# Performance work log

Measured on AMD Instinct MI355X. Metric: run time of the kernel, lower is better.

The kernel has to match this reference:

```python
import jax, jax.numpy as jnp
import numpy as np

B, T, C, L = 256, 512, 512, 64  # batch, timesteps, num_classes (blank = C-1), max label len
NEG = -1e30   # log-space 'minus infinity' that is safe under fp arithmetic
EPS = 1e-7    # keras.backend.epsilon() used by ctc_batch_cost


def _ctc_loss(log_probs, labels, in_len, lab_len, blank):
    """CTC negative log-likelihood via the forward (alpha) DP in log space.
    log_probs: [T, B, C] log probabilities; labels: [B, L] int; in_len, lab_len: [B] int.
    Returns [B] loss. Matches tf.nn.ctc_loss with merge_repeated=True, blank=C-1."""
    Tn, Bn, Cn = log_probs.shape
    Ln = labels.shape[1]
    S = 2 * Ln + 1  # extended label: blank, l1, blank, l2, ..., blank
    ext = jnp.full((Bn, S), blank, dtype=labels.dtype).at[:, 1::2].set(labels)  # [B,S]
    # skip transition s-2 -> s allowed iff ext[s] != blank and ext[s] != ext[s-2]
    allow = jnp.concatenate(
        [jnp.zeros((Bn, 2), dtype=bool),
         (ext[:, 2:] != blank) & (ext[:, 2:] != ext[:, :-2])], axis=1)  # [B,S]
    # emission log-probs for each extended-label position at every step: [T,B,S]
    emit = log_probs[:, jnp.arange(Bn)[:, None], ext]

    alpha0 = (jnp.full((Bn, S), NEG, dtype=log_probs.dtype)
              .at[:, 0].set(emit[0, :, 0])
              .at[:, 1].set(emit[0, :, 1]))

    def step(alpha, e):
        a1 = jnp.pad(alpha, ((0, 0), (1, 0)), constant_values=NEG)[:, :-1]
        a2 = jnp.pad(alpha, ((0, 0), (2, 0)), constant_values=NEG)[:, :-2]
        a2 = jnp.where(allow, a2, NEG)
        new = jax.nn.logsumexp(jnp.stack([alpha, a1, a2], axis=0), axis=0) + e
        return new, new

    _, alphas = jax.lax.scan(step, alpha0, emit[1:])
    alphas = jnp.concatenate([alpha0[None], alphas], axis=0)  # [T,B,S]
    # alpha at the last valid timestep of each sample
    final = alphas[in_len - 1, jnp.arange(Bn)]  # [B,S]
    i1 = (2 * lab_len)[:, None]       # last blank position
    i2 = (2 * lab_len - 1)[:, None]   # last label position
    last = jnp.concatenate(
        [jnp.take_along_axis(final, i1, axis=1),
         jnp.take_along_axis(final, i2, axis=1)], axis=1)  # [B,2]
    return -jax.nn.logsumexp(last, axis=1)  # [B]


def setup_inputs() -> dict:
    key = jax.random.key(0)
    k1, k2 = jax.random.split(key)
    # model output is a softmax distribution over classes (keras ctc_batch_cost contract)
    y_pred = jax.nn.softmax(jax.random.normal(k1, (B, T, C), dtype=jnp.float32), axis=-1)
    y_true = jax.random.randint(k2, (B, L), 0, C - 1, dtype=jnp.int32)  # never blank (C-1)
    input_length = jnp.full((B, 1), T, dtype=jnp.int32)
    label_length = jnp.full((B, 1), L, dtype=jnp.int32)
    return {"y_true": y_true, "y_pred": y_pred,
            "input_length": input_length, "label_length": label_length}


def reference(y_true, y_pred, input_length, label_length):
    # keras.backend.ctc_batch_cost: log(transpose(y_pred) + eps), blank = num_classes-1
    log_probs = jnp.log(jnp.transpose(y_pred, (1, 0, 2)) + EPS)  # [T,B,C]
    loss = _ctc_loss(log_probs, y_true, input_length[:, 0], label_length[:, 0], C - 1)
    return loss[:, None]  # [B,1], matching ctc_batch_cost
```

## Files before the change

### kernel.cpp

```cpp
#include <hip/hip_runtime.h>


constexpr int Bc = 256, Tc = 512, Cc = 512, Lc = 64;
constexpr int BLANK = Cc - 1;
constexpr float EPSF = 1e-7f;
constexpr float NEGI = -1e30f;
constexpr float LN2 = 0.6931471805599453f;
constexpr int K = 16;
constexpr int NC = (Tc - 1 + K - 1) / K;

__device__ __forceinline__ float exp2_hw(float x) { return __builtin_amdgcn_exp2f(x); }
__device__ __forceinline__ float log2_hw(float x) { return __builtin_amdgcn_logf(x); }

__device__ __forceinline__ float lse2(float a, float b) {
    float m = fmaxf(a, b);
    return m + log2_hw(exp2_hw(a - m) + exp2_hw(b - m));
}
__device__ __forceinline__ float lse3(float a, float b, float c) {
    float m = fmaxf(fmaxf(a, b), c);
    return m + log2_hw(exp2_hw(a - m) + exp2_hw(b - m) + exp2_hw(c - m));
}

__global__ __launch_bounds__(64, 1) void ctc_fwd(
    const int* __restrict__ labels,
    const float* __restrict__ yp,
    const int* __restrict__ in_len,
    const int* __restrict__ lab_len,
    float* __restrict__ out)
{
    const int b = blockIdx.x;
    const int lane = threadIdx.x;

    const float* __restrict__ row0 = yp + (size_t)b * (size_t)(Tc * Cc);

    const int lab = labels[b * Lc + lane];
    const int labPrev = __shfl_up(lab, 1);
    const bool allow = (lane >= 1 && lab != BLANK && lab != labPrev);

    int til = in_len[b];  if (til > Tc) til = Tc;
    const int lln = lab_len[b];

    float aB, aL, aH = NEGI;
    {
        float eb0 = log2_hw(row0[BLANK] + EPSF);
        float el0 = log2_hw(row0[lab] + EPSF);
        aB = (lane == 0) ? eb0 : NEGI;
        aL = (lane == 0) ? el0 : NEGI;
    }

    float curL[K], curB[K], nxtL[K], nxtB[K];

    auto loadChunk = [&](int c, float* dL, float* dB) {
        #pragma unroll
        for (int k = 0; k < K; ++k) {
            int t = 1 + c * K + k;
            bool v = (t < Tc);
            size_t o = (size_t)t * Cc;
            dL[k] = v ? row0[o + lab]   : 1.0f;
            dB[k] = v ? row0[o + BLANK] : 1.0f;
        }
    };

    loadChunk(0, curL, curB);

    for (int c = 0; c < NC; ++c) {
        if (c + 1 < NC) loadChunk(c + 1, nxtL, nxtB);

        #pragma unroll
        for (int k = 0; k < K; ++k) {
            int t = 1 + c * K + k;
            float el = log2_hw(curL[k] + EPSF);
            float eb = log2_hw(curB[k] + EPSF);

            float lp = __shfl_up(aL, 1);
            lp = (lane == 0) ? NEGI : lp;
            float lpm = allow ? lp : NEGI;

            float nB = lse2(aB, lp) + eb;
            float nL = lse3(aL, aB, lpm) + el;
            float nH = lse2(aH, aL) + eb;
            if (t < til) { aB = nB; aL = nL; aH = nH; }
        }

        #pragma unroll
        for (int k = 0; k < K; ++k) { curL[k] = nxtL[k]; curB[k] = nxtB[k]; }
    }

    float v1a = __shfl(aB, lln & 63);
    float v1b = __shfl(aH, 63);
    float v1 = (lln >= 64) ? v1b : v1a;
    float v2 = (lln >= 1) ? __shfl(aL, (lln - 1) & 63) : NEGI;

    if (lane == 0) out[b] = -LN2 * lse2(v1, v2);
}

extern "C" void kernel_launch(void* const* d_in, const int* in_sizes, int n_in,
                              void* d_out, int out_size, void* d_ws, size_t ws_size,
                              hipStream_t stream) {
    const int*   y_true       = (const int*)d_in[0];
    const float* y_pred       = (const float*)d_in[1];
    const int*   input_length = (const int*)d_in[2];
    const int*   label_length = (const int*)d_in[3];
    float*       out          = (float*)d_out;

    ctc_fwd<<<Bc, 64, 0, stream>>>(y_true, y_pred, input_length, label_length, out);
}
```

Measured before the change: 371.1 us.

## Warp-specialize CTC: producer waves prefetch log-emissions to LDS, one wave runs DP

Each block now holds 8 waves. Seven producer waves gather the label and blank probabilities for the next 64-timestep segment, take their logs, and write them into double-buffered shared memory, while wave 0 runs the serial alpha recursion from LDS. This moves global-load latency and the log computation off the DP critical path. The cost is a block-wide barrier every segment and a larger block, with one block per sample still giving 256 blocks.

After: 387.8 us. 1.04x slower.

```diff
diff --git a/kernel.cpp b/kernel.cpp
--- a/kernel.cpp
+++ b/kernel.cpp
@@ -6,8 +6,10 @@
 constexpr float EPSF = 1e-7f;
 constexpr float NEGI = -1e30f;
 constexpr float LN2 = 0.6931471805599453f;
-constexpr int K = 16;
-constexpr int NC = (Tc - 1 + K - 1) / K;
+constexpr int SR = 64;
+constexpr int NSEG = Tc / SR;
+constexpr int NW = 8;
+constexpr int NPROD = NW - 1;
 
 __device__ __forceinline__ float exp2_hw(float x) { return __builtin_amdgcn_exp2f(x); }
 __device__ __forceinline__ float log2_hw(float x) { return __builtin_amdgcn_logf(x); }
@@ -21,15 +23,20 @@
     return m + log2_hw(exp2_hw(a - m) + exp2_hw(b - m) + exp2_hw(c - m));
 }
 
-__global__ __launch_bounds__(64, 1) void ctc_fwd(
+__global__ __launch_bounds__(NW * 64, 1) void ctc_fwd(
     const int* __restrict__ labels,
     const float* __restrict__ yp,
     const int* __restrict__ in_len,
     const int* __restrict__ lab_len,
     float* __restrict__ out)
 {
+    __shared__ float sL[2][SR * 64];
+    __shared__ float sB[2][SR];
+
     const int b = blockIdx.x;
-    const int lane = threadIdx.x;
+    const int tid = threadIdx.x;
+    const int lane = tid & 63;
+    const int wave = tid >> 6;
 
     const float* __restrict__ row0 = yp + (size_t)b * (size_t)(Tc * Cc);
 
@@ -40,6 +47,16 @@
     int til = in_len[b];  if (til > Tc) til = Tc;
     const int lln = lab_len[b];
 
+    auto fillRow = [&](int buf, int t, int r) {
+        float v  = row0[(size_t)t * Cc + lab];
+        float vb = row0[(size_t)t * Cc + BLANK];
+        sL[buf][r * 64 + lane] = log2_hw(v + EPSF);
+        if (lane == 0) sB[buf][r] = log2_hw(vb + EPSF);
+    };
+
+    #pragma unroll 2
+    for (int r = wave; r < SR; r += NW) fillRow(0, r, r);
+
     float aB, aL, aH = NEGI;
     {
         float eb0 = log2_hw(row0[BLANK] + EPSF);
@@ -48,50 +65,41 @@
         aL = (lane == 0) ? el0 : NEGI;
     }
 
-    float curL[K], curB[K], nxtL[K], nxtB[K];
+    __syncthreads();
 
-    auto loadChunk = [&](int c, float* dL, float* dB) {
-        #pragma unroll
-        for (int k = 0; k < K; ++k) {
-            int t = 1 + c * K + k;
-            bool v = (t < Tc);
-            size_t o = (size_t)t * Cc;
-            dL[k] = v ? row0[o + lab]   : 1.0f;
-            dB[k] = v ? row0[o + BLANK] : 1.0f;
+    for (int s = 0; s < NSEG; ++s) {
+        const int buf = s & 1;
+        if (wave == 0) {
+            #pragma unroll 8
+            for (int k = 0; k < SR; ++k) {
+                int t = s * SR + k;
+                float el = sL[buf][k * 64 + lane];
+                float eb = sB[buf][k];
+
+                float lp = __shfl_up(aL, 1);
+                lp = (lane == 0) ? NEGI : lp;
+                float lpm = allow ? lp : NEGI;
+
+                float nB = lse2(aB, lp) + eb;
+                float nL = lse3(aL, aB, lpm) + el;
+                float nH = lse2(aH, aL) + eb;
+                if (t >= 1 && t < til) { aB = nB; aL = nL; aH = nH; }
+            }
+        } else if (s + 1 < NSEG) {
+            const int tb = (s + 1) * SR;
+            #pragma unroll 2
+            for (int r = wave - 1; r < SR; r += NPROD) fillRow(buf ^ 1, tb + r, r);
         }
-    };
-
-    loadChunk(0, curL, curB);
-
-    for (int c = 0; c < NC; ++c) {
-        if (c + 1 < NC) loadChunk(c + 1, nxtL, nxtB);
-
-        #pragma unroll
-        for (int k = 0; k < K; ++k) {
-            int t = 1 + c * K + k;
-            float el = log2_hw(curL[k] + EPSF);
-            float eb = log2_hw(curB[k] + EPSF);
-
-            float lp = __shfl_up(aL, 1);
-            lp = (lane == 0) ? NEGI : lp;
-            float lpm = allow ? lp : NEGI;
-
-            float nB = lse2(aB, lp) + eb;
-            float nL = lse3(aL, aB, lpm) + el;
-            float nH = lse2(aH, aL) + eb;
-            if (t < til) { aB = nB; aL = nL; aH = nH; }
-        }
-
-        #pragma unroll
-        for (int k = 0; k < K; ++k) { curL[k] = nxtL[k]; curB[k] = nxtB[k]; }
+        __syncthreads();
     }
 
-    float v1a = __shfl(aB, lln & 63);
-    float v1b = __shfl(aH, 63);
-    float v1 = (lln >= 64) ? v1b : v1a;
-    float v2 = (lln >= 1) ? __shfl(aL, (lln - 1) & 63) : NEGI;
-
-    if (lane == 0) out[b] = -LN2 * lse2(v1, v2);
+    if (wave == 0) {
+        float v1a = __shfl(aB, lln & 63);
+        float v1b = __shfl(aH, 63);
+        float v1 = (lln >= 64) ? v1b : v1a;
+        float v2 = (lln >= 1) ? __shfl(aL, (lln - 1) & 63) : NEGI;
+        if (lane == 0) out[b] = -LN2 * lse2(v1, v2);
+    }
 }
 
 extern "C" void kernel_launch(void* const* d_in, const int* in_sizes, int n_in,
@@ -103,5 +111,5 @@
     const int*   label_length = (const int*)d_in[3];
     float*       out          = (float*)d_out;
 
-    ctc_fwd<<<Bc, 64, 0, stream>>>(y_true, y_pred, input_length, label_length, out);
+    ctc_fwd<<<Bc, NW * 64, 0, stream>>>(y_true, y_pred, input_length, label_length, out);
 }
```
